# Kernel optimization log

Hardware: AMD Instinct MI355X
Metric: run time of the kernel (lower is better)

Reference implementation:

```python
import jax, jax.numpy as jnp
import numpy as np

N_NODES = 100000
N_EDGES = 1600000
D_IN = 64
D_OUT = 64


def setup_inputs() -> dict:
    key = jax.random.key(0)
    k1, k2, k3, k4, k5, k6 = jax.random.split(key, 6)
    x = jax.random.normal(k1, (N_NODES, D_IN), dtype=jnp.float32)
    edge_index = jax.random.randint(k2, (2, N_EDGES), 0, N_NODES, dtype=jnp.int64)
    edge_weight = jax.random.uniform(k3, (N_EDGES,), dtype=jnp.float32)
    scale = 1.0 / np.sqrt(D_IN)
    W0 = jax.random.normal(k4, (D_IN, D_OUT), dtype=jnp.float32) * scale
    W1 = jax.random.normal(k5, (D_IN, D_OUT), dtype=jnp.float32) * scale
    b = jax.random.normal(k6, (D_OUT,), dtype=jnp.float32) * 0.01
    return {"x": x, "edge_index": edge_index, "edge_weight": edge_weight,
            "W0": W0, "W1": W1, "b": b}


def reference(x, edge_index, edge_weight, W0, W1, b):
    # ChebConv K=2 with default lambda_max=2.0, sym normalization:
    # L_hat = 2L/lambda_max - I = -D^{-1/2} A D^{-1/2}
    N = x.shape[0]
    row, col = edge_index[0], edge_index[1]
    deg = jax.ops.segment_sum(edge_weight, row, num_segments=N)  # [N]
    deg_safe = jnp.where(deg > 0, deg, 1.0)
    dinv = jnp.where(deg > 0, jax.lax.rsqrt(deg_safe), 0.0)
    norm = -dinv[row] * edge_weight * dinv[col]  # [E], L_hat edge weights
    # Tx_1[i] = sum_{e: col_e = i} norm_e * x[row_e]
    Tx1 = jax.ops.segment_sum(norm[:, None] * x[row], col, num_segments=N)
    # out = lin0(Tx_0) + lin1(Tx_1) + bias
    return x @ W0 + Tx1 @ W1 + b
```

## Files before the change

### kernel.cpp

```cpp
#include <hip/hip_runtime.h>

#define N_NODES 100000
#define N_EDGES 1600000
#define D 64
#define NC 391
#define NCP 392
#define NBLK 128
#define EPB (N_EDGES / NBLK)
#define CAPC 5120
#define SCAP 768
#define AST 68

__device__ __forceinline__ unsigned bf16rne(float f) {
    unsigned u = __float_as_uint(f);
    return (u + 0x7FFFu + ((u >> 16) & 1u)) >> 16;
}
__global__ __launch_bounds__(256) void tobf16_kernel(const float* __restrict__ x,
                                                     ushort* __restrict__ xh,
                                                     float* __restrict__ deg4) {
    int id = blockIdx.x * 256 + threadIdx.x;
    if (id < 4 * N_NODES) deg4[id] = 0.f;
    int i = id * 8;
    float4 a = *(const float4*)(x + i);
    float4 b = *(const float4*)(x + i + 4);
    uint4 o;
    o.x = bf16rne(a.x) | (bf16rne(a.y) << 16);
    o.y = bf16rne(a.z) | (bf16rne(a.w) << 16);
    o.z = bf16rne(b.x) | (bf16rne(b.y) << 16);
    o.w = bf16rne(b.z) | (bf16rne(b.w) << 16);
    *(uint4*)(xh + i) = o;
}

__global__ __launch_bounds__(512) void countA_kernel(const int* __restrict__ row,
                                                     const int* __restrict__ col,
                                                     const float* __restrict__ w,
                                                     float* __restrict__ deg4,
                                                     int* __restrict__ cntA) {
    __shared__ int h[NCP];
    int t = threadIdx.x;
    for (int j = t; j < NCP; j += 512) h[j] = 0;
    __syncthreads();
    int base = blockIdx.x * EPB;
    float* dg = deg4 + (size_t)(blockIdx.x & 3) * N_NODES;
    for (int i = t; i < EPB; i += 512) {
        int e = base + i;
        atomicAdd(&dg[row[e]], w[e]);
        atomicAdd(&h[col[e] >> 8], 1);
    }
    __syncthreads();
    int* mc = cntA + (size_t)blockIdx.x * NCP;
    for (int j = t; j < NCP; j += 512) mc[j] = h[j];
}

__global__ __launch_bounds__(512) void scanA_kernel(int* __restrict__ cntA,
                                                    int* __restrict__ cbase) {
    __shared__ int tot[512];
    int t = threadIdx.x;
    int s = 0;
    if (t < NC)
        for (int b = 0; b < NBLK; ++b) s += cntA[(size_t)b * NCP + t];
    tot[t] = s;
    __syncthreads();
    for (int off = 1; off < 512; off <<= 1) {
        int u = (t >= off) ? tot[t - off] : 0;
        __syncthreads();
        tot[t] += u;
        __syncthreads();
    }
    int excl = (t > 0) ? tot[t - 1] : 0;
    if (t < NC) {
        cbase[t] = excl;
        int off2 = excl;
        for (int b = 0; b < NBLK; ++b) {
            int v = cntA[(size_t)b * NCP + t];
            cntA[(size_t)b * NCP + t] = off2;
            off2 += v;
        }
    }
    if (t == 0) cbase[NC] = N_EDGES;
}

__global__ __launch_bounds__(512) void scatterA_kernel(const int* __restrict__ row,
                                                       const int* __restrict__ col,
                                                       const float* __restrict__ w,
                                                       const int* __restrict__ offA,
                                                       int2* __restrict__ recA) {
    __shared__ int curs[NCP];
    int t = threadIdx.x;
    const int* oa = offA + (size_t)blockIdx.x * NCP;
    for (int j = t; j < NCP; j += 512) curs[j] = oa[j];
    __syncthreads();
    int base = blockIdx.x * EPB;
    for (int i = t; i < EPB; i += 512) {
        int e = base + i;
        int r = row[e];
        int c = col[e];
        float we = w[e];
        int p = atomicAdd(&curs[c >> 8], 1);
        recA[p] = make_int2(((c & 255) << 17) | r, __float_as_int(we));
    }
}

__global__ __launch_bounds__(256) void dinv_kernel(const float* __restrict__ deg4,
                                                   float* __restrict__ dinv) {
    int i = (blockIdx.x * 256 + threadIdx.x) * 4;
    if (i >= N_NODES) return;
    float4 a = *(const float4*)(deg4 + i);
    float4 b = *(const float4*)(deg4 + N_NODES + i);
    float4 c = *(const float4*)(deg4 + 2 * N_NODES + i);
    float4 d = *(const float4*)(deg4 + 3 * N_NODES + i);
    float4 o;
    float sx = a.x + b.x + c.x + d.x;
    float sy = a.y + b.y + c.y + d.y;
    float sz = a.z + b.z + c.z + d.z;
    float sw = a.w + b.w + c.w + d.w;
    o.x = sx > 0.f ? rsqrtf(sx) : 0.f;
    o.y = sy > 0.f ? rsqrtf(sy) : 0.f;
    o.z = sz > 0.f ? rsqrtf(sz) : 0.f;
    o.w = sw > 0.f ? rsqrtf(sw) : 0.f;
    *(float4*)(dinv + i) = o;
}

__global__ __launch_bounds__(256) void sortB_kernel(const int* __restrict__ cbase,
                                                    const float* __restrict__ dinv,
                                                    int2* __restrict__ recA,
                                                    int* __restrict__ node_start) {
    __shared__ int2 buf[CAPC];
    __shared__ int h[256];
    __shared__ int cu[256];
    __shared__ int wsum[4];
    int t = threadIdx.x;
    int cb = blockIdx.x;
    int base = cbase[cb];
    int cnt = min(cbase[cb + 1] - base, CAPC);
    h[t] = 0;
    __syncthreads();
    for (int i = t; i < cnt; i += 256)
        atomicAdd(&h[(recA[base + i].x >> 17) & 255], 1);
    __syncthreads();
    int v = h[t];
    int lane = t & 63, wv = t >> 6;
    int inc = v;
    #pragma unroll
    for (int d2 = 1; d2 < 64; d2 <<= 1) {
        int u = __shfl_up(inc, d2, 64);
        if (lane >= d2) inc += u;
    }
    if (lane == 63) wsum[wv] = inc;
    __syncthreads();
    int woff = 0;
    for (int w2 = 0; w2 < wv; ++w2) woff += wsum[w2];
    int st = woff + inc - v;
    cu[t] = st;
    int nid = cb * 256 + t;
    if (nid <= N_NODES) node_start[nid] = base + st;
    __syncthreads();
    for (int i = t; i < cnt; i += 256) {
        int2 rc = recA[base + i];
        int r = rc.x & 0x1FFFF;
        float cf = __int_as_float(rc.y) * dinv[r];
        int p = atomicAdd(&cu[(rc.x >> 17) & 255], 1);
        buf[p] = make_int2(r, __float_as_int(cf));
    }
    __syncthreads();
    for (int i = t; i < cnt; i += 256) recA[base + i] = buf[i];
}

#define FMA_BF16(e, u)                                                         \
    do { float cc = __int_as_float((e).y);                                     \
        acc0.x += cc * __uint_as_float((u).x << 16);                           \
        acc0.y += cc * __uint_as_float((u).x & 0xFFFF0000u);                   \
        acc0.z += cc * __uint_as_float((u).y << 16);                           \
        acc0.w += cc * __uint_as_float((u).y & 0xFFFF0000u);                   \
        acc1.x += cc * __uint_as_float((u).z << 16);                           \
        acc1.y += cc * __uint_as_float((u).z & 0xFFFF0000u);                   \
        acc1.z += cc * __uint_as_float((u).w << 16);                           \
        acc1.w += cc * __uint_as_float((u).w & 0xFFFF0000u);                   \
    } while (0)

__global__ __launch_bounds__(256, 8) void gather_out_kernel(
        const int2* __restrict__ recS, const int* __restrict__ node_start,
        const float* __restrict__ dinv, const ushort* __restrict__ xh,
        const float* __restrict__ x, const float* __restrict__ W0,
        const float* __restrict__ W1, const float* __restrict__ bias,
        float* __restrict__ out) {
    __shared__ __align__(16) char smemA[32 * AST * 4];
    __shared__ __align__(16) char smemB[32 * AST * 4];
    __shared__ int s33[33];
    int2*  stg = (int2*)smemA;
    float* xs  = (float*)smemA;
    float* ts  = (float*)smemB;

    int tid = threadIdx.x;
    int b   = blockIdx.x;
    int n0  = b * 32;
    int g   = tid >> 3;
    int j   = tid & 7;

    if (tid < 33) s33[tid] = node_start[n0 + tid];
    __syncthreads();
    int base = s33[0];
    int cnt  = s33[32] - base;
    int ks   = s33[g];
    int ke   = s33[g + 1];

    float4 acc0 = make_float4(0.f, 0.f, 0.f, 0.f);
    float4 acc1 = make_float4(0.f, 0.f, 0.f, 0.f);
    const ushort* xhj = xh + (j << 3);

    for (int off = 0; off < cnt; off += SCAP) {
        int m = min(SCAP, cnt - off);
        for (int i = tid; i < m; i += 256) stg[i] = recS[base + off + i];
        __syncthreads();
        int k0 = max(ks - base - off, 0);
        int k1 = min(ke - base - off, m);
        int k = k0;
        for (; k + 3 < k1; k += 4) {
            int2 e0 = stg[k + 0];
            int2 e1 = stg[k + 1];
            int2 e2 = stg[k + 2];
            int2 e3 = stg[k + 3];
            uint4 u0 = *(const uint4*)(xhj + ((size_t)e0.x << 6));
            uint4 u1 = *(const uint4*)(xhj + ((size_t)e1.x << 6));
            uint4 u2 = *(const uint4*)(xhj + ((size_t)e2.x << 6));
            uint4 u3 = *(const uint4*)(xhj + ((size_t)e3.x << 6));
            FMA_BF16(e0, u0);
            FMA_BF16(e1, u1);
            FMA_BF16(e2, u2);
            FMA_BF16(e3, u3);
        }
        for (; k < k1; ++k) {
            int2 e0 = stg[k];
            uint4 u0 = *(const uint4*)(xhj + ((size_t)e0.x << 6));
            FMA_BF16(e0, u0);
        }
        __syncthreads();
    }

    float dn = -dinv[n0 + g];
    float* tp = ts + g * AST + (j << 3);
    *(float4*)tp       = make_float4(dn * acc0.x, dn * acc0.y, dn * acc0.z, dn * acc0.w);
    *(float4*)(tp + 4) = make_float4(dn * acc1.x, dn * acc1.y, dn * acc1.z, dn * acc1.w);
    for (int i = tid; i < 512; i += 256) {
        int nn = i >> 4;
        int kk = (i & 15) << 2;
        *(float4*)&xs[nn * AST + kk] = *(const float4*)(x + (size_t)n0 * D + i * 4);
    }
    __syncthreads();

    int jl = j << 3;
    float4 o0 = *(const float4*)(bias + jl);
    float4 o1 = *(const float4*)(bias + jl + 4);
    for (int k2 = 0; k2 < D; k2 += 4) {
        float4 av = *(const float4*)&xs[g * AST + k2];
        float4 tv = *(const float4*)&ts[g * AST + k2];
        #pragma unroll
        for (int u = 0; u < 4; ++u) {
            float a = (u == 0) ? av.x : (u == 1) ? av.y : (u == 2) ? av.z : av.w;
            float t = (u == 0) ? tv.x : (u == 1) ? tv.y : (u == 2) ? tv.z : tv.w;
            const float4 w00 = *(const float4*)(W0 + (size_t)(k2 + u) * D + jl);
            const float4 w01 = *(const float4*)(W0 + (size_t)(k2 + u) * D + jl + 4);
            const float4 w10 = *(const float4*)(W1 + (size_t)(k2 + u) * D + jl);
            const float4 w11 = *(const float4*)(W1 + (size_t)(k2 + u) * D + jl + 4);
            o0.x += a * w00.x + t * w10.x;
            o0.y += a * w00.y + t * w10.y;
            o0.z += a * w00.z + t * w10.z;
            o0.w += a * w00.w + t * w10.w;
            o1.x += a * w01.x + t * w11.x;
            o1.y += a * w01.y + t * w11.y;
            o1.z += a * w01.z + t * w11.z;
            o1.w += a * w01.w + t * w11.w;
        }
    }
    float* op = out + (size_t)(n0 + g) * D + jl;
    *(float4*)op       = o0;
    *(float4*)(op + 4) = o1;
}

extern "C" void kernel_launch(void* const* d_in, const int* in_sizes, int n_in,
                              void* d_out, int out_size, void* d_ws, size_t ws_size,
                              hipStream_t stream) {
    const float* x    = (const float*)d_in[0];
    const int*   eidx = (const int*)d_in[1];
    const float* ew   = (const float*)d_in[2];
    const float* W0   = (const float*)d_in[3];
    const float* W1   = (const float*)d_in[4];
    const float* b    = (const float*)d_in[5];
    float* out = (float*)d_out;

    const int* row = eidx;
    const int* col = eidx + N_EDGES;

    int2*   recA  = (int2*)d_ws;
    int*    cntA  = (int*)(recA + N_EDGES);
    int*    cbase = cntA + (size_t)NBLK * NCP;
    float*  deg4  = (float*)(cbase + 400);
    float*  dinv  = deg4 + 4 * N_NODES;
    int*    node_start = (int*)(dinv + N_NODES);
    ushort* xh    = (ushort*)(node_start + 100016);

    tobf16_kernel  <<<N_NODES * D / (256 * 8), 256, 0, stream>>>(x, xh, deg4);
    countA_kernel  <<<NBLK, 512, 0, stream>>>(row, col, ew, deg4, cntA);
    scanA_kernel   <<<1, 512, 0, stream>>>(cntA, cbase);
    scatterA_kernel<<<NBLK, 512, 0, stream>>>(row, col, ew, cntA, recA);
    dinv_kernel    <<<(N_NODES / 4 + 255) / 256, 256, 0, stream>>>(deg4, dinv);
    sortB_kernel   <<<NC, 256, 0, stream>>>(cbase, dinv, recA, node_start);
    gather_out_kernel<<<N_NODES / 32, 256, 0, stream>>>(recA, node_start, dinv,
                                                        xh, x, W0, W1, b, out);
}
```

Measured before the change: 340.1 us.

## Parallelize bucket scan, fuse dinv into scan, drop LDS staging in gather

The single-block serial scan over per-block bucket counts is replaced. Counts are stored transposed, bucket totals are accumulated atomically, and a 391-block scan kernel computes per-bucket bases and per-block offsets with wave shuffles while also computing dinv, which removes the separate dinv kernel. NBLK doubles to 256 to give the counting and scatter passes more parallelism. The gather kernel now reads edge records directly from global memory instead of staging them through LDS with barriers, and uses two accumulator sets to break the FMA dependency chain.

```diff
diff --git a/kernel.cpp b/kernel.cpp
--- a/kernel.cpp
+++ b/kernel.cpp
@@ -5,10 +5,9 @@
 #define D 64
 #define NC 391
 #define NCP 392
-#define NBLK 128
-#define EPB (N_EDGES / NBLK)
+#define NBLK 256
+#define EPB 6250
 #define CAPC 5120
-#define SCAP 768
 #define AST 68
 
 __device__ __forceinline__ unsigned bf16rne(float f) {
@@ -17,9 +16,11 @@
 }
 __global__ __launch_bounds__(256) void tobf16_kernel(const float* __restrict__ x,
                                                      ushort* __restrict__ xh,
-                                                     float* __restrict__ deg4) {
+                                                     float* __restrict__ deg4,
+                                                     int* __restrict__ btot) {
     int id = blockIdx.x * 256 + threadIdx.x;
     if (id < 4 * N_NODES) deg4[id] = 0.f;
+    if (id < NC) btot[id] = 0;
     int i = id * 8;
     float4 a = *(const float4*)(x + i);
     float4 b = *(const float4*)(x + i + 4);
@@ -31,66 +32,87 @@
     *(uint4*)(xh + i) = o;
 }
 
-__global__ __launch_bounds__(512) void countA_kernel(const int* __restrict__ row,
-                                                     const int* __restrict__ col,
-                                                     const float* __restrict__ w,
-                                                     float* __restrict__ deg4,
-                                                     int* __restrict__ cntA) {
+__global__ __launch_bounds__(512) void countdeg_kernel(const int* __restrict__ row,
+                                                       const int* __restrict__ col,
+                                                       const float* __restrict__ w,
+                                                       float* __restrict__ deg4,
+                                                       int* __restrict__ cntT,
+                                                       int* __restrict__ btot) {
     __shared__ int h[NCP];
     int t = threadIdx.x;
+    int b = blockIdx.x;
     for (int j = t; j < NCP; j += 512) h[j] = 0;
     __syncthreads();
-    int base = blockIdx.x * EPB;
-    float* dg = deg4 + (size_t)(blockIdx.x & 3) * N_NODES;
+    int base = b * EPB;
+    float* dg = deg4 + (size_t)(b & 3) * N_NODES;
     for (int i = t; i < EPB; i += 512) {
         int e = base + i;
         atomicAdd(&dg[row[e]], w[e]);
         atomicAdd(&h[col[e] >> 8], 1);
     }
     __syncthreads();
-    int* mc = cntA + (size_t)blockIdx.x * NCP;
-    for (int j = t; j < NCP; j += 512) mc[j] = h[j];
-}
-
-__global__ __launch_bounds__(512) void scanA_kernel(int* __restrict__ cntA,
-                                                    int* __restrict__ cbase) {
-    __shared__ int tot[512];
+    for (int j = t; j < NC; j += 512) {
+        int v = h[j];
+        cntT[(size_t)j * NBLK + b] = v;
+        if (v) atomicAdd(&btot[j], v);
+    }
+}
+
+__global__ __launch_bounds__(512) void scanD_kernel(const int* __restrict__ btot,
+                                                    int* __restrict__ cbase,
+                                                    int* __restrict__ cntT,
+                                                    const float* __restrict__ deg4,
+                                                    float* __restrict__ dinv) {
+    __shared__ int sc[512];
+    __shared__ int wsum[8];
+    int j = blockIdx.x;
     int t = threadIdx.x;
-    int s = 0;
-    if (t < NC)
-        for (int b = 0; b < NBLK; ++b) s += cntA[(size_t)b * NCP + t];
-    tot[t] = s;
+    int bt = (t < NC) ? btot[t] : 0;
+    sc[t] = bt;
     __syncthreads();
     for (int off = 1; off < 512; off <<= 1) {
-        int u = (t >= off) ? tot[t - off] : 0;
+        int u = (t >= off) ? sc[t - off] : 0;
         __syncthreads();
-        tot[t] += u;
+        sc[t] += u;
         __syncthreads();
     }
-    int excl = (t > 0) ? tot[t - 1] : 0;
-    if (t < NC) {
-        cbase[t] = excl;
-        int off2 = excl;
-        for (int b = 0; b < NBLK; ++b) {
-            int v = cntA[(size_t)b * NCP + t];
-            cntA[(size_t)b * NCP + t] = off2;
-            off2 += v;
+    int cbv = sc[j] - btot[j];
+    if (t == 0) cbase[j] = cbv;
+    if (j == 0 && t == 0) cbase[NC] = N_EDGES;
+    int v = (t < NBLK) ? cntT[(size_t)j * NBLK + t] : 0;
+    int lane = t & 63, wv = t >> 6;
+    int inc = v;
+    #pragma unroll
+    for (int d = 1; d < 64; d <<= 1) {
+        int u = __shfl_up(inc, d, 64);
+        if (lane >= d) inc += u;
+    }
+    if (lane == 63) wsum[wv] = inc;
+    __syncthreads();
+    int woff = 0;
+    for (int w2 = 0; w2 < wv; ++w2) woff += wsum[w2];
+    if (t < NBLK) cntT[(size_t)j * NBLK + t] = cbv + woff + inc - v;
+    if (t < 256) {
+        int n = j * 256 + t;
+        if (n < N_NODES) {
+            float d = deg4[n] + deg4[N_NODES + n] + deg4[2 * N_NODES + n]
+                    + deg4[3 * N_NODES + n];
+            dinv[n] = d > 0.f ? rsqrtf(d) : 0.f;
         }
     }
-    if (t == 0) cbase[NC] = N_EDGES;
 }
 
 __global__ __launch_bounds__(512) void scatterA_kernel(const int* __restrict__ row,
                                                        const int* __restrict__ col,
                                                        const float* __restrict__ w,
-                                                       const int* __restrict__ offA,
+                                                       const int* __restrict__ cntT,
                                                        int2* __restrict__ recA) {
     __shared__ int curs[NCP];
     int t = threadIdx.x;
-    const int* oa = offA + (size_t)blockIdx.x * NCP;
-    for (int j = t; j < NCP; j += 512) curs[j] = oa[j];
-    __syncthreads();
-    int base = blockIdx.x * EPB;
+    int b = blockIdx.x;
+    for (int j = t; j < NC; j += 512) curs[j] = cntT[(size_t)j * NBLK + b];
+    __syncthreads();
+    int base = b * EPB;
     for (int i = t; i < EPB; i += 512) {
         int e = base + i;
         int r = row[e];
@@ -99,26 +121,6 @@
         int p = atomicAdd(&curs[c >> 8], 1);
         recA[p] = make_int2(((c & 255) << 17) | r, __float_as_int(we));
     }
-}
-
-__global__ __launch_bounds__(256) void dinv_kernel(const float* __restrict__ deg4,
-                                                   float* __restrict__ dinv) {
-    int i = (blockIdx.x * 256 + threadIdx.x) * 4;
-    if (i >= N_NODES) return;
-    float4 a = *(const float4*)(deg4 + i);
-    float4 b = *(const float4*)(deg4 + N_NODES + i);
-    float4 c = *(const float4*)(deg4 + 2 * N_NODES + i);
-    float4 d = *(const float4*)(deg4 + 3 * N_NODES + i);
-    float4 o;
-    float sx = a.x + b.x + c.x + d.x;
-    float sy = a.y + b.y + c.y + d.y;
-    float sz = a.z + b.z + c.z + d.z;
-    float sw = a.w + b.w + c.w + d.w;
-    o.x = sx > 0.f ? rsqrtf(sx) : 0.f;
-    o.y = sy > 0.f ? rsqrtf(sy) : 0.f;
-    o.z = sz > 0.f ? rsqrtf(sz) : 0.f;
-    o.w = sw > 0.f ? rsqrtf(sw) : 0.f;
-    *(float4*)(dinv + i) = o;
 }
 
 __global__ __launch_bounds__(256) void sortB_kernel(const int* __restrict__ cbase,
@@ -166,16 +168,16 @@
     for (int i = t; i < cnt; i += 256) recA[base + i] = buf[i];
 }
 
-#define FMA_BF16(e, u)                                                         \
+#define FMA_BF16T(e, u, A, B)                                                  \
     do { float cc = __int_as_float((e).y);                                     \
-        acc0.x += cc * __uint_as_float((u).x << 16);                           \
-        acc0.y += cc * __uint_as_float((u).x & 0xFFFF0000u);                   \
-        acc0.z += cc * __uint_as_float((u).y << 16);                           \
-        acc0.w += cc * __uint_as_float((u).y & 0xFFFF0000u);                   \
-        acc1.x += cc * __uint_as_float((u).z << 16);                           \
-        acc1.y += cc * __uint_as_float((u).z & 0xFFFF0000u);                   \
-        acc1.z += cc * __uint_as_float((u).w << 16);                           \
-        acc1.w += cc * __uint_as_float((u).w & 0xFFFF0000u);                   \
+        A.x += cc * __uint_as_float((u).x << 16);                              \
+        A.y += cc * __uint_as_float((u).x & 0xFFFF0000u);                      \
+        A.z += cc * __uint_as_float((u).y << 16);                              \
+        A.w += cc * __uint_as_float((u).y & 0xFFFF0000u);                      \
+        B.x += cc * __uint_as_float((u).z << 16);                              \
+        B.y += cc * __uint_as_float((u).z & 0xFFFF0000u);                      \
+        B.z += cc * __uint_as_float((u).w << 16);                              \
+        B.w += cc * __uint_as_float((u).w & 0xFFFF0000u);                      \
     } while (0)
 
 __global__ __launch_bounds__(256, 8) void gather_out_kernel(
@@ -184,12 +186,9 @@
         const float* __restrict__ x, const float* __restrict__ W0,
         const float* __restrict__ W1, const float* __restrict__ bias,
         float* __restrict__ out) {
-    __shared__ __align__(16) char smemA[32 * AST * 4];
-    __shared__ __align__(16) char smemB[32 * AST * 4];
+    __shared__ __align__(16) float xs[32 * AST];
+    __shared__ __align__(16) float ts[32 * AST];
     __shared__ int s33[33];
-    int2*  stg = (int2*)smemA;
-    float* xs  = (float*)smemA;
-    float* ts  = (float*)smemB;
 
     int tid = threadIdx.x;
     int b   = blockIdx.x;
@@ -199,43 +198,37 @@
 
     if (tid < 33) s33[tid] = node_start[n0 + tid];
     __syncthreads();
-    int base = s33[0];
-    int cnt  = s33[32] - base;
-    int ks   = s33[g];
-    int ke   = s33[g + 1];
-
-    float4 acc0 = make_float4(0.f, 0.f, 0.f, 0.f);
-    float4 acc1 = make_float4(0.f, 0.f, 0.f, 0.f);
+    int ks = s33[g];
+    int ke = s33[g + 1];
+
+    float4 p0 = make_float4(0.f, 0.f, 0.f, 0.f);
+    float4 p1 = make_float4(0.f, 0.f, 0.f, 0.f);
+    float4 q0 = make_float4(0.f, 0.f, 0.f, 0.f);
+    float4 q1 = make_float4(0.f, 0.f, 0.f, 0.f);
     const ushort* xhj = xh + (j << 3);
 
-    for (int off = 0; off < cnt; off += SCAP) {
-        int m = min(SCAP, cnt - off);
-        for (int i = tid; i < m; i += 256) stg[i] = recS[base + off + i];
-        __syncthreads();
-        int k0 = max(ks - base - off, 0);
-        int k1 = min(ke - base - off, m);
-        int k = k0;
-        for (; k + 3 < k1; k += 4) {
-            int2 e0 = stg[k + 0];
-            int2 e1 = stg[k + 1];
-            int2 e2 = stg[k + 2];
-            int2 e3 = stg[k + 3];
-            uint4 u0 = *(const uint4*)(xhj + ((size_t)e0.x << 6));
-            uint4 u1 = *(const uint4*)(xhj + ((size_t)e1.x << 6));
-            uint4 u2 = *(const uint4*)(xhj + ((size_t)e2.x << 6));
-            uint4 u3 = *(const uint4*)(xhj + ((size_t)e3.x << 6));
-            FMA_BF16(e0, u0);
-            FMA_BF16(e1, u1);
-            FMA_BF16(e2, u2);
-            FMA_BF16(e3, u3);
-        }
-        for (; k < k1; ++k) {
-            int2 e0 = stg[k];
-            uint4 u0 = *(const uint4*)(xhj + ((size_t)e0.x << 6));
-            FMA_BF16(e0, u0);
-        }
-        __syncthreads();
-    }
+    int k = ks;
+    for (; k + 3 < ke; k += 4) {
+        int2 e0 = recS[k + 0];
+        int2 e1 = recS[k + 1];
+        int2 e2 = recS[k + 2];
+        int2 e3 = recS[k + 3];
+        uint4 u0 = *(const uint4*)(xhj + ((size_t)e0.x << 6));
+        uint4 u1 = *(const uint4*)(xhj + ((size_t)e1.x << 6));
+        uint4 u2 = *(const uint4*)(xhj + ((size_t)e2.x << 6));
+        uint4 u3 = *(const uint4*)(xhj + ((size_t)e3.x << 6));
+        FMA_BF16T(e0, u0, p0, p1);
+        FMA_BF16T(e1, u1, q0, q1);
+        FMA_BF16T(e2, u2, p0, p1);
+        FMA_BF16T(e3, u3, q0, q1);
+    }
+    for (; k < ke; ++k) {
+        int2 e0 = recS[k];
+        uint4 u0 = *(const uint4*)(xhj + ((size_t)e0.x << 6));
+        FMA_BF16T(e0, u0, p0, p1);
+    }
+    float4 acc0 = make_float4(p0.x + q0.x, p0.y + q0.y, p0.z + q0.z, p0.w + q0.w);
+    float4 acc1 = make_float4(p1.x + q1.x, p1.y + q1.y, p1.z + q1.z, p1.w + q1.w);
 
     float dn = -dinv[n0 + g];
     float* tp = ts + g * AST + (j << 3);
@@ -292,19 +285,19 @@
     const int* col = eidx + N_EDGES;
 
     int2*   recA  = (int2*)d_ws;
-    int*    cntA  = (int*)(recA + N_EDGES);
-    int*    cbase = cntA + (size_t)NBLK * NCP;
+    int*    cntT  = (int*)(recA + N_EDGES);
+    int*    btot  = cntT + (size_t)NC * NBLK;
+    int*    cbase = btot + 400;
     float*  deg4  = (float*)(cbase + 400);
     float*  dinv  = deg4 + 4 * N_NODES;
     int*    node_start = (int*)(dinv + N_NODES);
     ushort* xh    = (ushort*)(node_start + 100016);
 
-    tobf16_kernel  <<<N_NODES * D / (256 * 8), 256, 0, stream>>>(x, xh, deg4);
-    countA_kernel  <<<NBLK, 512, 0, stream>>>(row, col, ew, deg4, cntA);
-    scanA_kernel   <<<1, 512, 0, stream>>>(cntA, cbase);
-    scatterA_kernel<<<NBLK, 512, 0, stream>>>(row, col, ew, cntA, recA);
-    dinv_kernel    <<<(N_NODES / 4 + 255) / 256, 256, 0, stream>>>(deg4, dinv);
-    sortB_kernel   <<<NC, 256, 0, stream>>>(cbase, dinv, recA, node_start);
+    tobf16_kernel   <<<N_NODES * D / (256 * 8), 256, 0, stream>>>(x, xh, deg4, btot);
+    countdeg_kernel <<<NBLK, 512, 0, stream>>>(row, col, ew, deg4, cntT, btot);
+    scanD_kernel    <<<NC, 512, 0, stream>>>(btot, cbase, cntT, deg4, dinv);
+    scatterA_kernel <<<NBLK, 512, 0, stream>>>(row, col, ew, cntT, recA);
+    sortB_kernel    <<<NC, 256, 0, stream>>>(cbase, dinv, recA, node_start);
     gather_out_kernel<<<N_NODES / 32, 256, 0, stream>>>(recA, node_start, dinv,
                                                         xh, x, W0, W1, b, out);
 }
```

New measurement: 343.9 us. About the same (+1.1%).

## Fuse preprocessing kernels into one persistent kernel with grid barriers

Applied to the files above, without the earlier changes.

Replaces the six preprocessing launches (bf16 conversion, degree/count, scan, scatter, dinv, per-bucket sort) with a single persistent kernel of 448 blocks separated by software grid barriers. The degree accumulation now spreads over all blocks into a single array instead of four partial copies, and the column-bucket scan is parallelised across warps instead of run in one block. This removes launch gaps and tail effects between stages, at the cost of barrier spin overhead, a required memset, and the risk of deadlock if all blocks cannot be co-resident.

```diff
diff --git a/kernel.cpp b/kernel.cpp
--- a/kernel.cpp
+++ b/kernel.cpp
@@ -5,165 +5,192 @@
 #define D 64
 #define NC 391
 #define NCP 392
-#define NBLK 128
-#define EPB (N_EDGES / NBLK)
+#define CBLK 128
+#define CEPB 12500
+#define PBLK 448
+#define PTHR 512
+#define DEPB 3572
 #define CAPC 5120
 #define SCAP 768
 #define AST 68
 
+__device__ __forceinline__ void gridbar(int* bar, int nblk) {
+    __threadfence();
+    __syncthreads();
+    if (threadIdx.x == 0) {
+        int gen = __hip_atomic_load(bar + 1, __ATOMIC_RELAXED, __HIP_MEMORY_SCOPE_AGENT);
+        int prev = __hip_atomic_fetch_add(bar, 1, __ATOMIC_ACQ_REL, __HIP_MEMORY_SCOPE_AGENT);
+        if (prev == nblk - 1) {
+            __hip_atomic_store(bar, 0, __ATOMIC_RELAXED, __HIP_MEMORY_SCOPE_AGENT);
+            __hip_atomic_fetch_add(bar + 1, 1, __ATOMIC_RELEASE, __HIP_MEMORY_SCOPE_AGENT);
+        } else {
+            while (__hip_atomic_load(bar + 1, __ATOMIC_ACQUIRE, __HIP_MEMORY_SCOPE_AGENT) == gen)
+                __builtin_amdgcn_s_sleep(8);
+        }
+    }
+    __syncthreads();
+    __threadfence();
+}
+
 __device__ __forceinline__ unsigned bf16rne(float f) {
     unsigned u = __float_as_uint(f);
     return (u + 0x7FFFu + ((u >> 16) & 1u)) >> 16;
 }
-__global__ __launch_bounds__(256) void tobf16_kernel(const float* __restrict__ x,
-                                                     ushort* __restrict__ xh,
-                                                     float* __restrict__ deg4) {
-    int id = blockIdx.x * 256 + threadIdx.x;
-    if (id < 4 * N_NODES) deg4[id] = 0.f;
-    int i = id * 8;
-    float4 a = *(const float4*)(x + i);
-    float4 b = *(const float4*)(x + i + 4);
-    uint4 o;
-    o.x = bf16rne(a.x) | (bf16rne(a.y) << 16);
-    o.y = bf16rne(a.z) | (bf16rne(a.w) << 16);
-    o.z = bf16rne(b.x) | (bf16rne(b.y) << 16);
-    o.w = bf16rne(b.z) | (bf16rne(b.w) << 16);
-    *(uint4*)(xh + i) = o;
-}
-
-__global__ __launch_bounds__(512) void countA_kernel(const int* __restrict__ row,
-                                                     const int* __restrict__ col,
-                                                     const float* __restrict__ w,
-                                                     float* __restrict__ deg4,
-                                                     int* __restrict__ cntA) {
-    __shared__ int h[NCP];
-    int t = threadIdx.x;
-    for (int j = t; j < NCP; j += 512) h[j] = 0;
-    __syncthreads();
-    int base = blockIdx.x * EPB;
-    float* dg = deg4 + (size_t)(blockIdx.x & 3) * N_NODES;
-    for (int i = t; i < EPB; i += 512) {
-        int e = base + i;
-        atomicAdd(&dg[row[e]], w[e]);
-        atomicAdd(&h[col[e] >> 8], 1);
-    }
-    __syncthreads();
-    int* mc = cntA + (size_t)blockIdx.x * NCP;
-    for (int j = t; j < NCP; j += 512) mc[j] = h[j];
-}
-
-__global__ __launch_bounds__(512) void scanA_kernel(int* __restrict__ cntA,
-                                                    int* __restrict__ cbase) {
-    __shared__ int tot[512];
-    int t = threadIdx.x;
-    int s = 0;
-    if (t < NC)
-        for (int b = 0; b < NBLK; ++b) s += cntA[(size_t)b * NCP + t];
-    tot[t] = s;
-    __syncthreads();
-    for (int off = 1; off < 512; off <<= 1) {
-        int u = (t >= off) ? tot[t - off] : 0;
-        __syncthreads();
-        tot[t] += u;
-        __syncthreads();
-    }
-    int excl = (t > 0) ? tot[t - 1] : 0;
-    if (t < NC) {
-        cbase[t] = excl;
-        int off2 = excl;
-        for (int b = 0; b < NBLK; ++b) {
-            int v = cntA[(size_t)b * NCP + t];
-            cntA[(size_t)b * NCP + t] = off2;
-            off2 += v;
-        }
-    }
-    if (t == 0) cbase[NC] = N_EDGES;
-}
-
-__global__ __launch_bounds__(512) void scatterA_kernel(const int* __restrict__ row,
-                                                       const int* __restrict__ col,
-                                                       const float* __restrict__ w,
-                                                       const int* __restrict__ offA,
-                                                       int2* __restrict__ recA) {
-    __shared__ int curs[NCP];
-    int t = threadIdx.x;
-    const int* oa = offA + (size_t)blockIdx.x * NCP;
-    for (int j = t; j < NCP; j += 512) curs[j] = oa[j];
-    __syncthreads();
-    int base = blockIdx.x * EPB;
-    for (int i = t; i < EPB; i += 512) {
-        int e = base + i;
-        int r = row[e];
-        int c = col[e];
-        float we = w[e];
-        int p = atomicAdd(&curs[c >> 8], 1);
-        recA[p] = make_int2(((c & 255) << 17) | r, __float_as_int(we));
-    }
-}
-
-__global__ __launch_bounds__(256) void dinv_kernel(const float* __restrict__ deg4,
-                                                   float* __restrict__ dinv) {
-    int i = (blockIdx.x * 256 + threadIdx.x) * 4;
-    if (i >= N_NODES) return;
-    float4 a = *(const float4*)(deg4 + i);
-    float4 b = *(const float4*)(deg4 + N_NODES + i);
-    float4 c = *(const float4*)(deg4 + 2 * N_NODES + i);
-    float4 d = *(const float4*)(deg4 + 3 * N_NODES + i);
-    float4 o;
-    float sx = a.x + b.x + c.x + d.x;
-    float sy = a.y + b.y + c.y + d.y;
-    float sz = a.z + b.z + c.z + d.z;
-    float sw = a.w + b.w + c.w + d.w;
-    o.x = sx > 0.f ? rsqrtf(sx) : 0.f;
-    o.y = sy > 0.f ? rsqrtf(sy) : 0.f;
-    o.z = sz > 0.f ? rsqrtf(sz) : 0.f;
-    o.w = sw > 0.f ? rsqrtf(sw) : 0.f;
-    *(float4*)(dinv + i) = o;
-}
-
-__global__ __launch_bounds__(256) void sortB_kernel(const int* __restrict__ cbase,
-                                                    const float* __restrict__ dinv,
-                                                    int2* __restrict__ recA,
-                                                    int* __restrict__ node_start) {
-    __shared__ int2 buf[CAPC];
-    __shared__ int h[256];
-    __shared__ int cu[256];
-    __shared__ int wsum[4];
-    int t = threadIdx.x;
-    int cb = blockIdx.x;
-    int base = cbase[cb];
-    int cnt = min(cbase[cb + 1] - base, CAPC);
-    h[t] = 0;
-    __syncthreads();
-    for (int i = t; i < cnt; i += 256)
-        atomicAdd(&h[(recA[base + i].x >> 17) & 255], 1);
-    __syncthreads();
-    int v = h[t];
-    int lane = t & 63, wv = t >> 6;
-    int inc = v;
-    #pragma unroll
-    for (int d2 = 1; d2 < 64; d2 <<= 1) {
-        int u = __shfl_up(inc, d2, 64);
-        if (lane >= d2) inc += u;
-    }
-    if (lane == 63) wsum[wv] = inc;
-    __syncthreads();
-    int woff = 0;
-    for (int w2 = 0; w2 < wv; ++w2) woff += wsum[w2];
-    int st = woff + inc - v;
-    cu[t] = st;
-    int nid = cb * 256 + t;
-    if (nid <= N_NODES) node_start[nid] = base + st;
-    __syncthreads();
-    for (int i = t; i < cnt; i += 256) {
-        int2 rc = recA[base + i];
-        int r = rc.x & 0x1FFFF;
-        float cf = __int_as_float(rc.y) * dinv[r];
-        int p = atomicAdd(&cu[(rc.x >> 17) & 255], 1);
-        buf[p] = make_int2(r, __float_as_int(cf));
-    }
-    __syncthreads();
-    for (int i = t; i < cnt; i += 256) recA[base + i] = buf[i];
+
+__global__ __launch_bounds__(512, 4) void fused_pre(
+        const float* __restrict__ x, const int* __restrict__ row,
+        const int* __restrict__ col, const float* __restrict__ w,
+        ushort* __restrict__ xh, float* __restrict__ deg,
+        int* __restrict__ cntC, int* __restrict__ btot, int* __restrict__ cbase,
+        float* __restrict__ dinv, int2* __restrict__ recA,
+        int* __restrict__ node_start, int* __restrict__ bar) {
+    __shared__ __align__(16) char smem[43072];
+    int tid = threadIdx.x;
+    int b   = blockIdx.x;
+    int gid = b * PTHR + tid;
+    const int NT = PBLK * PTHR;
+
+    for (int i = gid; i < N_NODES * D / 8; i += NT) {
+        int ii = i * 8;
+        float4 a  = *(const float4*)(x + ii);
+        float4 b4 = *(const float4*)(x + ii + 4);
+        uint4 o;
+        o.x = bf16rne(a.x)  | (bf16rne(a.y)  << 16);
+        o.y = bf16rne(a.z)  | (bf16rne(a.w)  << 16);
+        o.z = bf16rne(b4.x) | (bf16rne(b4.y) << 16);
+        o.w = bf16rne(b4.z) | (bf16rne(b4.w) << 16);
+        *(uint4*)(xh + ii) = o;
+    }
+    for (int i = gid; i < N_NODES; i += NT) deg[i] = 0.f;
+    if (gid < NC) btot[gid] = 0;
+    gridbar(bar, PBLK);
+
+    {
+        int base = b * DEPB;
+        for (int i = tid; i < DEPB; i += PTHR) {
+            int e = base + i;
+            if (e < N_EDGES) atomicAdd(&deg[row[e]], w[e]);
+        }
+    }
+    if (b < CBLK) {
+        int* h = (int*)smem;
+        for (int j = tid; j < NCP; j += PTHR) h[j] = 0;
+        __syncthreads();
+        int base = b * CEPB;
+        for (int i = tid; i < CEPB; i += PTHR) atomicAdd(&h[col[base + i] >> 8], 1);
+        __syncthreads();
+        int* mc = cntC + (size_t)b * NCP;
+        for (int j = tid; j < NC; j += PTHR) {
+            int v = h[j];
+            mc[j] = v;
+            if (v) atomicAdd(&btot[j], v);
+        }
+    }
+    gridbar(bar, PBLK);
+
+    for (int i = gid; i < N_NODES; i += NT) {
+        float dd = deg[i];
+        dinv[i] = dd > 0.f ? rsqrtf(dd) : 0.f;
+    }
+    {
+        int* sc = (int*)smem;
+        int v = (tid < NC) ? btot[tid] : 0;
+        sc[tid] = v;
+        __syncthreads();
+        for (int off = 1; off < 512; off <<= 1) {
+            int u = (tid >= off) ? sc[tid - off] : 0;
+            __syncthreads();
+            sc[tid] += u;
+            __syncthreads();
+        }
+        if (b == 0) {
+            if (tid < NC) cbase[tid] = sc[tid] - v;
+            if (tid == 0) cbase[NC] = N_EDGES;
+        }
+        int wv = tid >> 6, lane = tid & 63;
+        for (int j = b * 8 + wv; j < NC; j += PBLK * 8) {
+            int cbj = sc[j] - btot[j];
+            int t0 = lane * 2;
+            int v0 = cntC[(size_t)t0 * NCP + j];
+            int v1 = cntC[(size_t)(t0 + 1) * NCP + j];
+            int s = v0 + v1;
+            int inc = s;
+            #pragma unroll
+            for (int d2 = 1; d2 < 64; d2 <<= 1) {
+                int u = __shfl_up(inc, d2, 64);
+                if (lane >= d2) inc += u;
+            }
+            int excl = cbj + inc - s;
+            cntC[(size_t)t0 * NCP + j] = excl;
+            cntC[(size_t)(t0 + 1) * NCP + j] = excl + v0;
+        }
+    }
+    gridbar(bar, PBLK);
+
+    if (b < CBLK) {
+        int* curs = (int*)smem;
+        const int* mc = cntC + (size_t)b * NCP;
+        for (int j = tid; j < NC; j += PTHR) curs[j] = mc[j];
+        __syncthreads();
+        int base = b * CEPB;
+        for (int i = tid; i < CEPB; i += PTHR) {
+            int e = base + i;
+            int r = row[e];
+            int c = col[e];
+            float we = w[e];
+            int p = atomicAdd(&curs[c >> 8], 1);
+            recA[p] = make_int2(((c & 255) << 17) | r, __float_as_int(we));
+        }
+    }
+    gridbar(bar, PBLK);
+
+    {
+        int2* buf  = (int2*)smem;
+        int*  h    = (int*)(smem + CAPC * 8);
+        int*  cu   = h + 256;
+        int*  wsum = cu + 256;
+        for (int cb = b; cb < NC; cb += PBLK) {
+            int base = cbase[cb];
+            int cnt = min(cbase[cb + 1] - base, CAPC);
+            if (tid < 256) h[tid] = 0;
+            __syncthreads();
+            for (int i = tid; i < cnt; i += PTHR)
+                atomicAdd(&h[(recA[base + i].x >> 17) & 255], 1);
+            __syncthreads();
+            int v = 0, inc = 0;
+            if (tid < 256) {
+                v = h[tid];
+                inc = v;
+                int lane = tid & 63;
+                #pragma unroll
+                for (int d2 = 1; d2 < 64; d2 <<= 1) {
+                    int u = __shfl_up(inc, d2, 64);
+                    if (lane >= d2) inc += u;
+                }
+                if (lane == 63) wsum[tid >> 6] = inc;
+            }
+            __syncthreads();
+            if (tid < 256) {
+                int woff = 0;
+                for (int w2 = 0; w2 < (tid >> 6); ++w2) woff += wsum[w2];
+                int st = woff + inc - v;
+                cu[tid] = st;
+                int nid = cb * 256 + tid;
+                if (nid <= N_NODES) node_start[nid] = base + st;
+            }
+            __syncthreads();
+            for (int i = tid; i < cnt; i += PTHR) {
+                int2 rc = recA[base + i];
+                int r = rc.x & 0x1FFFF;
+                float cf = __int_as_float(rc.y) * dinv[r];
+                int p = atomicAdd(&cu[(rc.x >> 17) & 255], 1);
+                buf[p] = make_int2(r, __float_as_int(cf));
+            }
+            __syncthreads();
+            for (int i = tid; i < cnt; i += PTHR) recA[base + i] = buf[i];
+            __syncthreads();
+        }
+    }
 }
 
 #define FMA_BF16(e, u)                                                         \
@@ -292,19 +319,18 @@
     const int* col = eidx + N_EDGES;
 
     int2*   recA  = (int2*)d_ws;
-    int*    cntA  = (int*)(recA + N_EDGES);
-    int*    cbase = cntA + (size_t)NBLK * NCP;
-    float*  deg4  = (float*)(cbase + 400);
-    float*  dinv  = deg4 + 4 * N_NODES;
+    int*    cntC  = (int*)(recA + N_EDGES);
+    int*    btot  = cntC + (size_t)CBLK * NCP;
+    int*    cbase = btot + 400;
+    int*    bar   = cbase + 400;
+    float*  deg   = (float*)(bar + 4);
+    float*  dinv  = deg + N_NODES;
     int*    node_start = (int*)(dinv + N_NODES);
     ushort* xh    = (ushort*)(node_start + 100016);
 
-    tobf16_kernel  <<<N_NODES * D / (256 * 8), 256, 0, stream>>>(x, xh, deg4);
-    countA_kernel  <<<NBLK, 512, 0, stream>>>(row, col, ew, deg4, cntA);
-    scanA_kernel   <<<1, 512, 0, stream>>>(cntA, cbase);
-    scatterA_kernel<<<NBLK, 512, 0, stream>>>(row, col, ew, cntA, recA);
-    dinv_kernel    <<<(N_NODES / 4 + 255) / 256, 256, 0, stream>>>(deg4, dinv);
-    sortB_kernel   <<<NC, 256, 0, stream>>>(cbase, dinv, recA, node_start);
+    hipMemsetAsync(bar, 0, 2 * sizeof(int), stream);
+    fused_pre<<<PBLK, PTHR, 0, stream>>>(x, row, col, ew, xh, deg, cntC, btot,
+                                         cbase, dinv, recA, node_start, bar);
     gather_out_kernel<<<N_NODES / 32, 256, 0, stream>>>(recA, node_start, dinv,
                                                         xh, x, W0, W1, b, out);
 }
```

Result: slower. 1.301 ms (+282.5%).
